# Optimization experiments

Hardware: AMD Instinct MI355X
Metric: run time of the kernel (lower is better)

The kernel has to match this reference:

```python
import jax, jax.numpy as jnp
import numpy as np

B, IN_DIM, OUT_DIM, DEPTH = 8192, 4096, 2048, 9


def setup_inputs() -> dict:
    key = jax.random.key(0)
    k1, k2, k3, k4 = jax.random.split(key, 4)
    return {
        "x": jax.random.normal(k1, (B, IN_DIM), dtype=jnp.float32),
        "universal_weights": jax.random.normal(k2, (DEPTH, IN_DIM, OUT_DIM), dtype=jnp.float32),
        "classical_weights": jax.random.normal(k3, (IN_DIM, OUT_DIM), dtype=jnp.float32),
        "classical_biases": jax.random.normal(k4, (OUT_DIM,), dtype=jnp.float32),
    }


def _universal_probs(universal_weights, out_dim, in_dim):
    # Angles: original indexes universal_weights[depth, j, c] with j over output
    # dims and c in {0,1,2} (consciousness/intelligence/wisdom gates per depth).
    # Build the scan sequence in (depth, gate) order: shape (3*DEPTH, O).
    A = jnp.transpose(universal_weights[:, :out_dim, :3], (0, 2, 1)).reshape(-1, out_dim)
    # Initial state ones/sqrt(n), one independent state per output channel: (O, n)
    s0 = jnp.full((out_dim, in_dim), 1.0 / np.sqrt(in_dim), dtype=universal_weights.dtype)

    def step(s, ang):
        # Circulant tridiagonal rotation: diag=cos, super(+wrap)=-sin, sub(+wrap)=sin
        c = jnp.cos(ang)[:, None]
        sn = jnp.sin(ang)[:, None]
        s_next = c * s - sn * jnp.roll(s, -1, axis=1) + sn * jnp.roll(s, 1, axis=1)
        return s_next, None

    s, _ = jax.lax.scan(step, s0, A)
    # probability = |state[0]|^2 ; state is real so this is just the square
    return s[:, 0] ** 2  # (O,)


def reference(x, universal_weights, classical_weights, classical_biases):
    out_dim = classical_weights.shape[1]
    in_dim = x.shape[1]
    classical = x @ classical_weights + classical_biases  # (B, O)
    # Universal output is independent of the batch row (loop over i is dead code)
    probs = _universal_probs(universal_weights, out_dim, in_dim)  # (O,)
    return jnp.tanh(classical + probs[None, :])
```

## Files before the change

kernel.cpp:

```cpp
#include <hip/hip_runtime.h>
#include <cstdint>
#include <cstddef>

#define MM 8192
#define KK 4096
#define NN 2048
#define DEPTH_N 9

typedef __attribute__((ext_vector_type(8))) short bf16x8;
typedef __attribute__((ext_vector_type(16))) float f32x16;

static_assert(sizeof(bf16x8) == 16, "bf16x8 must be 16B");
static_assert(sizeof(f32x16) == 64, "f32x16 must be 64B");

typedef const __attribute__((address_space(1))) uint32_t* gptr_t;
typedef __attribute__((address_space(3))) uint32_t* lptr_t;

__device__ __forceinline__ void load_lds16(const void* g, void* l) {
  __builtin_amdgcn_global_load_lds((gptr_t)g, (lptr_t)l, 16, 0, 0);
}

union FragU {
  uint32_t u[4];
  bf16x8 v;
};

__device__ __forceinline__ void split4(float4 v, uint32_t& h01, uint32_t& h23,
                                       uint32_t& l01, uint32_t& l23) {
  uint32_t ux = __float_as_uint(v.x), uy = __float_as_uint(v.y);
  uint32_t uz = __float_as_uint(v.z), uw = __float_as_uint(v.w);
  h01 = __builtin_amdgcn_perm(uy, ux, 0x07060302u);
  h23 = __builtin_amdgcn_perm(uw, uz, 0x07060302u);
  float rx = v.x - __uint_as_float(ux & 0xFFFF0000u);
  float ry = v.y - __uint_as_float(uy & 0xFFFF0000u);
  float rz = v.z - __uint_as_float(uz & 0xFFFF0000u);
  float rw = v.w - __uint_as_float(uw & 0xFFFF0000u);
  l01 = __builtin_amdgcn_perm(__float_as_uint(ry), __float_as_uint(rx), 0x07060302u);
  l23 = __builtin_amdgcn_perm(__float_as_uint(rw), __float_as_uint(rz), 0x07060302u);
}

__global__ __launch_bounds__(256) void prep_bt_kernel(
    const float* __restrict__ W,
    uint16_t* __restrict__ btHi,
    uint16_t* __restrict__ btLo) {
  __shared__ float tile[64][65];
  const int k0 = blockIdx.x * 64;
  const int n0 = blockIdx.y * 64;
  const int c4 = (threadIdx.x & 15) * 4;
  const int r16 = threadIdx.x >> 4;
#pragma unroll
  for (int p = 0; p < 4; ++p) {
    int r = p * 16 + r16;
    float4 v = *(const float4*)(W + (size_t)(k0 + r) * NN + n0 + c4);
    tile[r][c4 + 0] = v.x;
    tile[r][c4 + 1] = v.y;
    tile[r][c4 + 2] = v.z;
    tile[r][c4 + 3] = v.w;
  }
  __syncthreads();
#pragma unroll
  for (int p = 0; p < 4; ++p) {
    int n = p * 16 + r16;
    ushort4 h, l;
    float f0 = tile[c4 + 0][n];
    float f1 = tile[c4 + 1][n];
    float f2 = tile[c4 + 2][n];
    float f3 = tile[c4 + 3][n];
    uint32_t u0 = __float_as_uint(f0), u1 = __float_as_uint(f1);
    uint32_t u2 = __float_as_uint(f2), u3 = __float_as_uint(f3);
    h.x = (uint16_t)(u0 >> 16);
    h.y = (uint16_t)(u1 >> 16);
    h.z = (uint16_t)(u2 >> 16);
    h.w = (uint16_t)(u3 >> 16);
    float r0 = f0 - __uint_as_float(u0 & 0xFFFF0000u);
    float r1 = f1 - __uint_as_float(u1 & 0xFFFF0000u);
    float r2 = f2 - __uint_as_float(u2 & 0xFFFF0000u);
    float r3 = f3 - __uint_as_float(u3 & 0xFFFF0000u);
    l.x = (uint16_t)(__float_as_uint(r0) >> 16);
    l.y = (uint16_t)(__float_as_uint(r1) >> 16);
    l.z = (uint16_t)(__float_as_uint(r2) >> 16);
    l.w = (uint16_t)(__float_as_uint(r3) >> 16);
    size_t off = (size_t)(n0 + n) * KK + k0 + c4;
    *(ushort4*)(btHi + off) = h;
    *(ushort4*)(btLo + off) = l;
  }
}

__global__ __launch_bounds__(256) void prep_bias_kernel(
    const float* __restrict__ uw,
    const float* __restrict__ cb,
    float* __restrict__ bias2) {
  int j = blockIdx.x * 256 + threadIdx.x;
  float p = 1.0f / (float)KK;
#pragma unroll
  for (int d = 0; d < DEPTH_N; ++d) {
    float4 v = *(const float4*)(uw + (size_t)d * KK * NN + (size_t)j * NN);
    float c0 = cosf(v.x), c1 = cosf(v.y), c2 = cosf(v.z);
    p *= (c0 * c0) * (c1 * c1) * (c2 * c2);
  }
  bias2[j] = cb[j] + p;
}

__global__ __launch_bounds__(256, 4) void unl_gemm_kernel(
    const float* __restrict__ X,
    const uint16_t* __restrict__ BtHi,
    const uint16_t* __restrict__ BtLo,
    const float* __restrict__ bias2,
    float* __restrict__ Out) {
  __shared__ __align__(16) uint8_t smem[32768];
  char* sA = (char*)smem;
  char* sBh = (char*)smem + 16384;
  char* sBl = (char*)smem + 24576;

  const int tid = threadIdx.x;
  const int lane = tid & 63;
  const int wq = __builtin_amdgcn_readfirstlane(tid >> 6);
  const int wM = wq >> 1;
  const int wN = wq & 1;
  const int lane31 = lane & 31;
  const int kh = lane >> 5;

  const int bidx = blockIdx.x;
  const int m0 = (bidx & 63) * 128;
  const int n0 = (bidx >> 6) * 128;

  const int aC = (lane & 7) ^ (lane >> 3);
  const int aVoff = ((lane >> 3) * KK + aC * 4) * 4;
  const char* aBase = (const char*)(X + (size_t)(m0 + wq * 32) * KK) + aVoff;
  const int bC = (lane & 3) ^ ((lane >> 3) & 3);
  const int bVoff = ((lane >> 2) * KK + bC * 8) * 2;
  const char* bBaseH = (const char*)(BtHi + (size_t)(n0 + wq * 32) * KK) + bVoff;
  const char* bBaseL = (const char*)(BtLo + (size_t)(n0 + wq * 32) * KK) + bVoff;

  int aOffB[2][2];
#pragma unroll
  for (int mt = 0; mt < 2; ++mt) {
    int row = wM * 64 + mt * 32 + lane31;
#pragma unroll
    for (int s = 0; s < 2; ++s)
      aOffB[mt][s] = row * 128 + (((4 * s + 2 * kh) ^ (row & 7)) * 16);
  }
  int bOffB[2][2];
#pragma unroll
  for (int nt = 0; nt < 2; ++nt) {
    int row = wN * 64 + nt * 32 + lane31;
#pragma unroll
    for (int s = 0; s < 2; ++s)
      bOffB[nt][s] = row * 64 + (((2 * s + kh) ^ ((row >> 1) & 3)) * 16);
  }

  f32x16 acc[2][2];
#pragma unroll
  for (int mt = 0; mt < 2; ++mt)
#pragma unroll
    for (int nt = 0; nt < 2; ++nt)
#pragma unroll
      for (int r = 0; r < 16; ++r) acc[mt][nt][r] = 0.0f;

  for (int kt = 0; kt < KK; kt += 32) {
    __syncthreads();
#pragma unroll
    for (int q = 0; q < 4; ++q)
      load_lds16(aBase + (size_t)kt * 4 + (size_t)q * (8 * KK * 4),
                 sA + (wq * 4 + q) * 1024);
#pragma unroll
    for (int q = 0; q < 2; ++q) {
      load_lds16(bBaseH + (size_t)kt * 2 + (size_t)q * (16 * KK * 2),
                 sBh + (wq * 2 + q) * 1024);
      load_lds16(bBaseL + (size_t)kt * 2 + (size_t)q * (16 * KK * 2),
                 sBl + (wq * 2 + q) * 1024);
    }
    __syncthreads();

#pragma unroll
    for (int s = 0; s < 2; ++s) {
      bf16x8 ah[2], al[2], bh[2], bl[2];
#pragma unroll
      for (int mt = 0; mt < 2; ++mt) {
        float4 v0 = *(const float4*)(sA + aOffB[mt][s]);
        float4 v1 = *(const float4*)(sA + (aOffB[mt][s] ^ 16));
        FragU uh, ul;
        split4(v0, uh.u[0], uh.u[1], ul.u[0], ul.u[1]);
        split4(v1, uh.u[2], uh.u[3], ul.u[2], ul.u[3]);
        ah[mt] = uh.v;
        al[mt] = ul.v;
      }
#pragma unroll
      for (int nt = 0; nt < 2; ++nt) {
        bh[nt] = *(const bf16x8*)(sBh + bOffB[nt][s]);
        bl[nt] = *(const bf16x8*)(sBl + bOffB[nt][s]);
      }
#pragma unroll
      for (int mt = 0; mt < 2; ++mt) {
#pragma unroll
        for (int nt = 0; nt < 2; ++nt) {
          acc[mt][nt] = __builtin_amdgcn_mfma_f32_32x32x16_bf16(ah[mt], bh[nt], acc[mt][nt], 0, 0, 0);
          acc[mt][nt] = __builtin_amdgcn_mfma_f32_32x32x16_bf16(ah[mt], bl[nt], acc[mt][nt], 0, 0, 0);
          acc[mt][nt] = __builtin_amdgcn_mfma_f32_32x32x16_bf16(al[mt], bh[nt], acc[mt][nt], 0, 0, 0);
        }
      }
    }
  }

#pragma unroll
  for (int nt = 0; nt < 2; ++nt) {
    int col = n0 + wN * 64 + nt * 32 + lane31;
    float b2 = bias2[col];
#pragma unroll
    for (int mt = 0; mt < 2; ++mt) {
#pragma unroll
      for (int r = 0; r < 16; ++r) {
        int rowl = (r & 3) + 8 * (r >> 2) + 4 * kh;
        int grow = m0 + wM * 64 + mt * 32 + rowl;
        float z = acc[mt][nt][r] + b2;
        z = fminf(fmaxf(z, -12.0f), 12.0f);
        float t = __expf(2.0f * z);
        Out[(size_t)grow * NN + col] = (t - 1.0f) / (t + 1.0f);
      }
    }
  }
}

extern "C" void kernel_launch(void* const* d_in, const int* in_sizes, int n_in,
                              void* d_out, int out_size, void* d_ws, size_t ws_size,
                              hipStream_t stream) {
  const float* x = (const float*)d_in[0];
  const float* uw = (const float*)d_in[1];
  const float* cw = (const float*)d_in[2];
  const float* cb = (const float*)d_in[3];
  float* out = (float*)d_out;

  uint16_t* btHi = (uint16_t*)d_ws;
  uint16_t* btLo = btHi + (size_t)NN * KK;
  float* bias2 = (float*)(btLo + (size_t)NN * KK);

  prep_bt_kernel<<<dim3(KK / 64, NN / 64), 256, 0, stream>>>(cw, btHi, btLo);
  prep_bias_kernel<<<dim3(NN / 256), 256, 0, stream>>>(uw, cb, bias2);
  unl_gemm_kernel<<<dim3((MM / 128) * (NN / 128)), 256, 0, stream>>>(x, btHi, btLo, bias2, out);
}
```

Before: 814.0 us.

## Pre-split activations into bf16 hi/lo in fused prep kernel before GEMM

```diff
diff --git a/kernel.cpp b/kernel.cpp
--- a/kernel.cpp
+++ b/kernel.cpp
@@ -39,15 +39,14 @@
   l23 = __builtin_amdgcn_perm(__float_as_uint(rw), __float_as_uint(rz), 0x07060302u);
 }
 
-__global__ __launch_bounds__(256) void prep_bt_kernel(
+__device__ __forceinline__ void prep_bt_body(
+    int k0, int n0, int tid,
     const float* __restrict__ W,
     uint16_t* __restrict__ btHi,
-    uint16_t* __restrict__ btLo) {
-  __shared__ float tile[64][65];
-  const int k0 = blockIdx.x * 64;
-  const int n0 = blockIdx.y * 64;
-  const int c4 = (threadIdx.x & 15) * 4;
-  const int r16 = threadIdx.x >> 4;
+    uint16_t* __restrict__ btLo,
+    float (*tile)[65]) {
+  const int c4 = (tid & 15) * 4;
+  const int r16 = tid >> 4;
 #pragma unroll
   for (int p = 0; p < 4; ++p) {
     int r = p * 16 + r16;
@@ -86,11 +85,9 @@
   }
 }
 
-__global__ __launch_bounds__(256) void prep_bias_kernel(
-    const float* __restrict__ uw,
-    const float* __restrict__ cb,
+__device__ __forceinline__ void prep_bias_body(
+    int j, const float* __restrict__ uw, const float* __restrict__ cb,
     float* __restrict__ bias2) {
-  int j = blockIdx.x * 256 + threadIdx.x;
   float p = 1.0f / (float)KK;
 #pragma unroll
   for (int d = 0; d < DEPTH_N; ++d) {
@@ -101,7 +98,162 @@
   bias2[j] = cb[j] + p;
 }
 
-__global__ __launch_bounds__(256, 4) void unl_gemm_kernel(
+#define PREP_A_BLOCKS (MM * KK / 4 / 256)
+#define PREP_BT_BLOCKS ((KK / 64) * (NN / 64))
+
+__global__ __launch_bounds__(256) void prep_fused_kernel(
+    const float* __restrict__ X,
+    const float* __restrict__ W,
+    const float* __restrict__ uw,
+    const float* __restrict__ cb,
+    uint16_t* __restrict__ aHi,
+    uint16_t* __restrict__ aLo,
+    uint16_t* __restrict__ btHi,
+    uint16_t* __restrict__ btLo,
+    float* __restrict__ bias2) {
+  __shared__ float tile[64][65];
+  const int bid = blockIdx.x;
+  const int tid = threadIdx.x;
+  if (bid < PREP_A_BLOCKS) {
+    size_t idx = (size_t)bid * 256 + tid;
+    float4 v = *(const float4*)(X + idx * 4);
+    uint32_t h01, h23, l01, l23;
+    split4(v, h01, h23, l01, l23);
+    ((uint2*)aHi)[idx] = make_uint2(h01, h23);
+    ((uint2*)aLo)[idx] = make_uint2(l01, l23);
+  } else if (bid < PREP_A_BLOCKS + PREP_BT_BLOCKS) {
+    int b = bid - PREP_A_BLOCKS;
+    prep_bt_body((b & 63) * 64, (b >> 6) * 64, tid, W, btHi, btLo, tile);
+  } else {
+    int j = (bid - PREP_A_BLOCKS - PREP_BT_BLOCKS) * 256 + tid;
+    prep_bias_body(j, uw, cb, bias2);
+  }
+}
+
+__global__ __launch_bounds__(256) void prep_bt_kernel(
+    const float* __restrict__ W, uint16_t* __restrict__ btHi,
+    uint16_t* __restrict__ btLo) {
+  __shared__ float tile[64][65];
+  prep_bt_body(blockIdx.x * 64, blockIdx.y * 64, threadIdx.x, W, btHi, btLo, tile);
+}
+
+__global__ __launch_bounds__(256) void prep_bias_kernel(
+    const float* __restrict__ uw, const float* __restrict__ cb,
+    float* __restrict__ bias2) {
+  prep_bias_body(blockIdx.x * 256 + threadIdx.x, uw, cb, bias2);
+}
+
+__global__ __launch_bounds__(256, 4) void unl_gemm_presplit_kernel(
+    const uint16_t* __restrict__ AHi,
+    const uint16_t* __restrict__ ALo,
+    const uint16_t* __restrict__ BtHi,
+    const uint16_t* __restrict__ BtLo,
+    const float* __restrict__ bias2,
+    float* __restrict__ Out) {
+  __shared__ __align__(16) uint8_t smem[32768];
+  char* sAh = (char*)smem;
+  char* sAl = (char*)smem + 8192;
+  char* sBh = (char*)smem + 16384;
+  char* sBl = (char*)smem + 24576;
+
+  const int tid = threadIdx.x;
+  const int lane = tid & 63;
+  const int wq = __builtin_amdgcn_readfirstlane(tid >> 6);
+  const int wM = wq >> 1;
+  const int wN = wq & 1;
+  const int lane31 = lane & 31;
+  const int kh = lane >> 5;
+
+  const int bidx = blockIdx.x;
+  const int m0 = (bidx & 63) * 128;
+  const int n0 = (bidx >> 6) * 128;
+
+  const int stC = (lane & 3) ^ ((lane >> 3) & 3);
+  const int stOff = ((lane >> 2) * KK + stC * 8) * 2;
+  const char* aBaseH = (const char*)(AHi + (size_t)(m0 + wq * 32) * KK) + stOff;
+  const char* aBaseL = (const char*)(ALo + (size_t)(m0 + wq * 32) * KK) + stOff;
+  const char* bBaseH = (const char*)(BtHi + (size_t)(n0 + wq * 32) * KK) + stOff;
+  const char* bBaseL = (const char*)(BtLo + (size_t)(n0 + wq * 32) * KK) + stOff;
+
+  int aOffB[2][2], bOffB[2][2];
+#pragma unroll
+  for (int t = 0; t < 2; ++t) {
+    int rowA = wM * 64 + t * 32 + lane31;
+    int rowB = wN * 64 + t * 32 + lane31;
+#pragma unroll
+    for (int s = 0; s < 2; ++s) {
+      aOffB[t][s] = rowA * 64 + (((2 * s + kh) ^ ((rowA >> 1) & 3)) * 16);
+      bOffB[t][s] = rowB * 64 + (((2 * s + kh) ^ ((rowB >> 1) & 3)) * 16);
+    }
+  }
+
+  f32x16 acc[2][2];
+#pragma unroll
+  for (int mt = 0; mt < 2; ++mt)
+#pragma unroll
+    for (int nt = 0; nt < 2; ++nt)
+#pragma unroll
+      for (int r = 0; r < 16; ++r) acc[mt][nt][r] = 0.0f;
+
+  for (int kt = 0; kt < KK; kt += 32) {
+    __syncthreads();
+    const size_t kb = (size_t)kt * 2;
+#pragma unroll
+    for (int q = 0; q < 2; ++q) {
+      const size_t qb = (size_t)q * (16 * KK * 2);
+      char* ldsOff = (char*)0 + (wq * 2 + q) * 1024;
+      load_lds16(aBaseH + kb + qb, sAh + (size_t)ldsOff);
+      load_lds16(aBaseL + kb + qb, sAl + (size_t)ldsOff);
+      load_lds16(bBaseH + kb + qb, sBh + (size_t)ldsOff);
+      load_lds16(bBaseL + kb + qb, sBl + (size_t)ldsOff);
+    }
+    __syncthreads();
+
+#pragma unroll
+    for (int s = 0; s < 2; ++s) {
+      bf16x8 ah[2], al[2], bh[2], bl[2];
+#pragma unroll
+      for (int mt = 0; mt < 2; ++mt) {
+        ah[mt] = *(const bf16x8*)(sAh + aOffB[mt][s]);
+        al[mt] = *(const bf16x8*)(sAl + aOffB[mt][s]);
+      }
+#pragma unroll
+      for (int nt = 0; nt < 2; ++nt) {
+        bh[nt] = *(const bf16x8*)(sBh + bOffB[nt][s]);
+        bl[nt] = *(const bf16x8*)(sBl + bOffB[nt][s]);
+      }
+#pragma unroll
+      for (int mt = 0; mt < 2; ++mt) {
+#pragma unroll
+        for (int nt = 0; nt < 2; ++nt) {
+          acc[mt][nt] = __builtin_amdgcn_mfma_f32_32x32x16_bf16(ah[mt], bh[nt], acc[mt][nt], 0, 0, 0);
+          acc[mt][nt] = __builtin_amdgcn_mfma_f32_32x32x16_bf16(ah[mt], bl[nt], acc[mt][nt], 0, 0, 0);
+          acc[mt][nt] = __builtin_amdgcn_mfma_f32_32x32x16_bf16(al[mt], bh[nt], acc[mt][nt], 0, 0, 0);
+        }
+      }
+    }
+  }
+
+#pragma unroll
+  for (int nt = 0; nt < 2; ++nt) {
+    int col = n0 + wN * 64 + nt * 32 + lane31;
+    float b2 = bias2[col];
+#pragma unroll
+    for (int mt = 0; mt < 2; ++mt) {
+#pragma unroll
+      for (int r = 0; r < 16; ++r) {
+        int rowl = (r & 3) + 8 * (r >> 2) + 4 * kh;
+        int grow = m0 + wM * 64 + mt * 32 + rowl;
+        float z = acc[mt][nt][r] + b2;
+        z = fminf(fmaxf(z, -12.0f), 12.0f);
+        float t = __expf(2.0f * z);
+        Out[(size_t)grow * NN + col] = (t - 1.0f) / (t + 1.0f);
+      }
+    }
+  }
+}
+
+__global__ __launch_bounds__(256, 4) void unl_gemm_fp32a_kernel(
     const float* __restrict__ X,
     const uint16_t* __restrict__ BtHi,
     const uint16_t* __restrict__ BtLo,
@@ -233,8 +385,19 @@
   uint16_t* btHi = (uint16_t*)d_ws;
   uint16_t* btLo = btHi + (size_t)NN * KK;
   float* bias2 = (float*)(btLo + (size_t)NN * KK);
-
-  prep_bt_kernel<<<dim3(KK / 64, NN / 64), 256, 0, stream>>>(cw, btHi, btLo);
-  prep_bias_kernel<<<dim3(NN / 256), 256, 0, stream>>>(uw, cb, bias2);
-  unl_gemm_kernel<<<dim3((MM / 128) * (NN / 128)), 256, 0, stream>>>(x, btHi, btLo, bias2, out);
-}
+  uint16_t* aHi = (uint16_t*)(bias2 + 2048);
+  uint16_t* aLo = aHi + (size_t)MM * KK;
+  const size_t need = (size_t)NN * KK * 4 + 2048 * 4 + (size_t)MM * KK * 4;
+
+  if (ws_size >= need) {
+    prep_fused_kernel<<<dim3(PREP_A_BLOCKS + PREP_BT_BLOCKS + NN / 256), 256, 0,
+                        stream>>>(x, cw, uw, cb, aHi, aLo, btHi, btLo, bias2);
+    unl_gemm_presplit_kernel<<<dim3((MM / 128) * (NN / 128)), 256, 0, stream>>>(
+        aHi, aLo, btHi, btLo, bias2, out);
+  } else {
+    prep_bt_kernel<<<dim3(KK / 64, NN / 64), 256, 0, stream>>>(cw, btHi, btLo);
+    prep_bias_kernel<<<dim3(NN / 256), 256, 0, stream>>>(uw, cb, bias2);
+    unl_gemm_fp32a_kernel<<<dim3((MM / 128) * (NN / 128)), 256, 0, stream>>>(
+        x, btHi, btLo, bias2, out);
+  }
+}
```

Result: slower. 863.1 us (+6.0%).
